# Kernel tuning notes

Measured on AMD Instinct MI355X. Metric: run time of the kernel, lower is better.

Reference implementation:

```python
import jax, jax.numpy as jnp
import numpy as np

B, S, D = 8, 2048, 64
NEG = -1e9


def setup_inputs() -> dict:
    key = jax.random.key(0)
    kq, kk, kv = jax.random.split(key, 3)
    return {
        "queries": jax.random.normal(kq, (B, S, D), dtype=jnp.float32),
        "keys": jax.random.normal(kk, (B, S, D), dtype=jnp.float32),
        "values": jax.random.normal(kv, (B, S, D), dtype=jnp.float32),
        "mask_q": jnp.ones((B, S), dtype=jnp.float32),
        "mask_k": jnp.ones((B, S), dtype=jnp.float32),
        "mask_v": jnp.ones((B, S), dtype=jnp.float32),
    }


def reference(queries, keys, values, mask_q, mask_k, mask_v):
    # scaled QK^T: [B, Sq, Sk]
    scaler = jnp.sqrt(jnp.asarray(queries.shape[-1], dtype=queries.dtype))
    scores = jnp.einsum("bqd,bkd->bqk", queries, keys) / scaler
    # additive padding mask from outer product of query/key masks
    padding_mask = mask_q[:, :, None] * mask_k[:, None, :]  # [B, Sq, Sk]
    scores = scores + (1.0 - padding_mask) * NEG
    attention_weights = jax.nn.softmax(scores, axis=-1)
    # mask values then weighted sum
    values = values * mask_v[:, :, None]
    output = jnp.einsum("bqk,bkd->bqd", attention_weights, values)
    return output
```

## Files before the change

### kernel.cpp

```cpp
#include <hip/hip_runtime.h>
#include <hip/hip_bf16.h>
#include <math.h>

#define BATCH 8
#define SEQ   2048
#define DIM   64
#define NEGC  (-1e9f)

typedef short short8 __attribute__((ext_vector_type(8)));
typedef float f32x4  __attribute__((ext_vector_type(4)));

#define MFMA(a, b, c) __builtin_amdgcn_mfma_f32_16x16x32_bf16((a), (b), (c), 0, 0, 0)

__device__ __forceinline__ ushort f2bf(float x) {
    uint u = __float_as_uint(x);
    uint r = (u + 0x7fffu + ((u >> 16) & 1u)) >> 16;
    return (ushort)r;
}
__device__ __forceinline__ float bf2f(ushort h) {
    return __uint_as_float(((uint)h) << 16);
}

__global__ __launch_bounds__(256)
void prep_kv(const float* __restrict__ K, const float* __restrict__ V,
             const float* __restrict__ MV, ushort* __restrict__ ws) {
    __shared__ float raw[64 * 68];
    const int t    = threadIdx.x;
    const int b    = blockIdx.x >> 5;
    const int tile = blockIdx.x & 31;
    const float* Kb  = K  + ((size_t)b * SEQ + tile * 64) * DIM;
    const float* Vb  = V  + ((size_t)b * SEQ + tile * 64) * DIM;
    const float* MVb = MV + (size_t)b * SEQ + tile * 64;
    ushort* wsI = ws + (size_t)(b * 32 + tile) * 8192;

#pragma unroll
    for (int u = 0; u < 4; u++) {
        int f = t + 256 * u, key = f >> 4, d4 = (f & 15) * 4;
        *(float4*)&raw[key * 68 + d4] = *(const float4*)(Kb + (size_t)f * 4);
    }
    __syncthreads();
#pragma unroll
    for (int u = 0; u < 2; u++) {
        int r = t + 256 * u;
        int mtc = r >> 6, qd = (r >> 4) & 3, mm = r & 15;
        int mt = mtc >> 1, c = mtc & 1;
        int key = mt * 16 + mm, d0 = c * 32 + qd * 8;
        float4 x0 = *(float4*)&raw[key * 68 + d0];
        float4 x1 = *(float4*)&raw[key * 68 + d0 + 4];
        float xs[8] = {x0.x, x0.y, x0.z, x0.w, x1.x, x1.y, x1.z, x1.w};
        short8 hv;
#pragma unroll
        for (int j = 0; j < 8; j++) hv[j] = (short)f2bf(xs[j]);
        *(short8*)(wsI + r * 8) = hv;
    }
    __syncthreads();

#pragma unroll
    for (int u = 0; u < 4; u++) {
        int f = t + 256 * u, key = f >> 4, d4 = (f & 15) * 4;
        float4 x = *(const float4*)(Vb + (size_t)f * 4);
        float mv = MVb[key];
        x.x *= mv; x.y *= mv; x.z *= mv; x.w *= mv;
        *(float4*)&raw[key * 68 + d4] = x;
    }
    __syncthreads();
#pragma unroll
    for (int u = 0; u < 2; u++) {
        int r = t + 256 * u;
        int kg5 = r >> 8, dg = (r >> 6) & 3, kq = (r >> 4) & 3, dm = r & 15;
        int d = dg * 16 + dm, k0 = kg5 * 32 + kq * 8;
        short8 ov;
#pragma unroll
        for (int j = 0; j < 8; j++) ov[j] = (short)f2bf(raw[(k0 + j) * 68 + d]);
        *(short8*)(wsI + 4096 + r * 8) = ov;
    }
}

__global__ __launch_bounds__(512, 2)
void attn_main(const float* __restrict__ Q, const float* __restrict__ MQ,
               const float* __restrict__ MK, const ushort* __restrict__ ws,
               float* __restrict__ O) {
    __shared__ __align__(16) ushort Stage[2][8192];
    __shared__ __align__(16) ushort Pf[8][512];
    __shared__ __align__(16) float  Msc[4][1280];

    const int t    = threadIdx.x;
    const int w    = t >> 6;
    const int lane = t & 63;
    const int quad = lane >> 4;
    const int lq   = lane & 15;
    const int qg   = w & 3;
    const int half = w >> 2;

    const int b  = blockIdx.x >> 5;
    const int q0 = (blockIdx.x & 31) * 64;
    const int q  = q0 + qg * 16 + lq;

    const float*  MKb = MK + (size_t)b * SEQ;
    const ushort* wsb = ws + (size_t)b * 32 * 8192;

    short8 qh[2], ql[2];
    {
        const float* Qr = Q + ((size_t)b * SEQ + q) * DIM;
#pragma unroll
        for (int c = 0; c < 2; c++) {
            float4 x0 = *(const float4*)(Qr + c * 32 + quad * 8);
            float4 x1 = *(const float4*)(Qr + c * 32 + quad * 8 + 4);
            float xs[8] = {x0.x, x0.y, x0.z, x0.w, x1.x, x1.y, x1.z, x1.w};
#pragma unroll
            for (int j = 0; j < 8; j++) {
                float v   = xs[j] * 0.125f;
                ushort hi = f2bf(v);
                ql[c][j]  = (short)f2bf(v - bf2f(hi));
                qh[c][j]  = (short)hi;
            }
        }
    }
    const float mq   = MQ[(size_t)b * SEQ + q];
    const float apen = NEGC * mq;

    float m = -1e30f, l = 0.0f;
    f32x4 ot0 = {0,0,0,0}, ot1 = {0,0,0,0}, ot2 = {0,0,0,0}, ot3 = {0,0,0,0};

    ushort* Pw   = Pf[w];
    const int kb = half * 32;

#pragma unroll
    for (int u = 0; u < 2; u++) {
        const int off = u * 4096 + w * 512;
        __builtin_amdgcn_global_load_lds(
            (const __attribute__((address_space(1))) void*)(wsb + off + lane * 8),
            (__attribute__((address_space(3))) void*)(&Stage[0][0] + off),
            16, 0, 0);
    }
    __syncthreads();

    f32x4 mkA = *(const f32x4*)(MKb + kb + quad * 4);
    f32x4 mkB = *(const f32x4*)(MKb + kb + 16 + quad * 4);

#pragma unroll 1
    for (int tile = 0; tile < 32; tile++) {
        const ushort* cur = &Stage[tile & 1][0];

        if (tile + 1 < 32) {
            const ushort* src = wsb + (size_t)(tile + 1) * 8192;
            ushort* dst = &Stage[(tile + 1) & 1][0];
#pragma unroll
            for (int u = 0; u < 2; u++) {
                const int off = u * 4096 + w * 512;
                __builtin_amdgcn_global_load_lds(
                    (const __attribute__((address_space(1))) void*)(src + off + lane * 8),
                    (__attribute__((address_space(3))) void*)(dst + off),
                    16, 0, 0);
            }
        }
        f32x4 nA = mkA, nB = mkB;
        if (tile + 1 < 32) {
            const float* mkp = MKb + (tile + 1) * 64 + kb + quad * 4;
            nA = *(const f32x4*)mkp;
            nB = *(const f32x4*)(mkp + 16);
        }

        f32x4 st0 = {0,0,0,0}, st1 = {0,0,0,0};
        const int mtg = half * 2;
#pragma unroll
        for (int c = 0; c < 2; c++) {
            short8 a0 = *(const short8*)&cur[((mtg + 0) * 2 + c) * 512 + lane * 8];
            short8 a1 = *(const short8*)&cur[((mtg + 1) * 2 + c) * 512 + lane * 8];
            st0 = MFMA(a0, qh[c], st0);
            st0 = MFMA(a0, ql[c], st0);
            st1 = MFMA(a1, qh[c], st1);
            st1 = MFMA(a1, ql[c], st1);
        }

        float s0[4], s1[4];
#pragma unroll
        for (int r = 0; r < 4; r++) {
            s0[r] = st0[r] + (NEGC - apen * mkA[r]);
            s1[r] = st1[r] + (NEGC - apen * mkB[r]);
        }
        float cm = s0[0];
#pragma unroll
        for (int r = 1; r < 4; r++) cm = fmaxf(cm, s0[r]);
#pragma unroll
        for (int r = 0; r < 4; r++) cm = fmaxf(cm, s1[r]);
        cm = fmaxf(cm, __shfl_xor(cm, 16));
        cm = fmaxf(cm, __shfl_xor(cm, 32));
        float nm    = fmaxf(m, cm);
        float alpha = __expf(m - nm);
        m = nm;

        float p0[4], p1[4], cs = 0.0f;
#pragma unroll
        for (int r = 0; r < 4; r++) { p0[r] = __expf(s0[r] - nm); cs += p0[r]; }
#pragma unroll
        for (int r = 0; r < 4; r++) { p1[r] = __expf(s1[r] - nm); cs += p1[r]; }
        cs += __shfl_xor(cs, 16);
        cs += __shfl_xor(cs, 32);
        l   = l * alpha + cs;
        ot0 *= alpha; ot1 *= alpha; ot2 *= alpha; ot3 *= alpha;

        __hip_bfloat162 c0 = __float22bfloat162_rn(make_float2(p0[0], p0[1]));
        __hip_bfloat162 c1 = __float22bfloat162_rn(make_float2(p0[2], p0[3]));
        __hip_bfloat162 c2 = __float22bfloat162_rn(make_float2(p1[0], p1[1]));
        __hip_bfloat162 c3 = __float22bfloat162_rn(make_float2(p1[2], p1[3]));
        uint2 pw0, pw1;
        __builtin_memcpy(&pw0.x, &c0, 4);
        __builtin_memcpy(&pw0.y, &c1, 4);
        __builtin_memcpy(&pw1.x, &c2, 4);
        __builtin_memcpy(&pw1.y, &c3, 4);
        int pidx0 = ((0 * 2 + (quad >> 1)) * 16 + lq) * 8 + (quad & 1) * 4;
        int pidx1 = ((1 * 2 + (quad >> 1)) * 16 + lq) * 8 + (quad & 1) * 4;
        *(uint2*)&Pw[pidx0] = pw0;
        *(uint2*)&Pw[pidx1] = pw1;
        short8 pfr = *(const short8*)&Pw[lane * 8];

        const ushort* VfC = cur + 4096;
        short8 v0 = *(const short8*)&VfC[(half * 4 + 0) * 512 + lane * 8];
        short8 v1 = *(const short8*)&VfC[(half * 4 + 1) * 512 + lane * 8];
        short8 v2 = *(const short8*)&VfC[(half * 4 + 2) * 512 + lane * 8];
        short8 v3 = *(const short8*)&VfC[(half * 4 + 3) * 512 + lane * 8];
        ot0 = MFMA(v0, pfr, ot0);
        ot1 = MFMA(v1, pfr, ot1);
        ot2 = MFMA(v2, pfr, ot2);
        ot3 = MFMA(v3, pfr, ot3);

        mkA = nA; mkB = nB;
        __syncthreads();
    }

    if (half == 1) {
        float* sc = &Msc[qg][lane * 20];
        *(f32x4*)&sc[0]  = ot0;
        *(f32x4*)&sc[4]  = ot1;
        *(f32x4*)&sc[8]  = ot2;
        *(f32x4*)&sc[12] = ot3;
        sc[16] = m;
        sc[17] = l;
    }
    __syncthreads();
    if (half == 0) {
        const float* sc = &Msc[qg][lane * 20];
        f32x4 ob0 = *(const f32x4*)&sc[0];
        f32x4 ob1 = *(const f32x4*)&sc[4];
        f32x4 ob2 = *(const f32x4*)&sc[8];
        f32x4 ob3 = *(const f32x4*)&sc[12];
        float mb = sc[16], lb = sc[17];

        float nm  = fmaxf(m, mb);
        float fa  = __expf(m - nm);
        float fb  = __expf(mb - nm);
        float inv = 1.0f / (l * fa + lb * fb);

        float* Orow = O + ((size_t)b * SEQ + q) * DIM;
        *(f32x4*)(Orow + 0  + quad * 4) = (ot0 * fa + ob0 * fb) * inv;
        *(f32x4*)(Orow + 16 + quad * 4) = (ot1 * fa + ob1 * fb) * inv;
        *(f32x4*)(Orow + 32 + quad * 4) = (ot2 * fa + ob2 * fb) * inv;
        *(f32x4*)(Orow + 48 + quad * 4) = (ot3 * fa + ob3 * fb) * inv;
    }
}

extern "C" void kernel_launch(void* const* d_in, const int* in_sizes, int n_in,
                              void* d_out, int out_size, void* d_ws, size_t ws_size,
                              hipStream_t stream) {
    const float* Q  = (const float*)d_in[0];
    const float* K  = (const float*)d_in[1];
    const float* V  = (const float*)d_in[2];
    const float* MQ = (const float*)d_in[3];
    const float* MK = (const float*)d_in[4];
    const float* MV = (const float*)d_in[5];
    float* O   = (float*)d_out;
    ushort* ws = (ushort*)d_ws;

    prep_kv<<<dim3(256), dim3(256), 0, stream>>>(K, V, MV, ws);
    attn_main<<<dim3(BATCH * (SEQ / 64)), dim3(512), 0, stream>>>(Q, MQ, MK, ws, O);
}
```

Before: 108.5 us.

## Switch to 32x32x16 MFMA, split keys across blocks, add merge kernel

```diff
diff --git a/kernel.cpp b/kernel.cpp
--- a/kernel.cpp
+++ b/kernel.cpp
@@ -7,10 +7,11 @@
 #define DIM   64
 #define NEGC  (-1e9f)
 
-typedef short short8 __attribute__((ext_vector_type(8)));
-typedef float f32x4  __attribute__((ext_vector_type(4)));
-
-#define MFMA(a, b, c) __builtin_amdgcn_mfma_f32_16x16x32_bf16((a), (b), (c), 0, 0, 0)
+typedef short short8  __attribute__((ext_vector_type(8)));
+typedef float f32x4   __attribute__((ext_vector_type(4)));
+typedef float f32x16  __attribute__((ext_vector_type(16)));
+
+#define MFMA32(a, b, c) __builtin_amdgcn_mfma_f32_32x32x16_bf16((a), (b), (c), 0, 0, 0)
 
 __device__ __forceinline__ ushort f2bf(float x) {
     uint u = __float_as_uint(x);
@@ -42,9 +43,8 @@
 #pragma unroll
     for (int u = 0; u < 2; u++) {
         int r = t + 256 * u;
-        int mtc = r >> 6, qd = (r >> 4) & 3, mm = r & 15;
-        int mt = mtc >> 1, c = mtc & 1;
-        int key = mt * 16 + mm, d0 = c * 32 + qd * 8;
+        int mt = r >> 8, kc = (r >> 6) & 3, L = r & 63;
+        int key = mt * 32 + (L & 31), d0 = kc * 16 + (L >> 5) * 8;
         float4 x0 = *(float4*)&raw[key * 68 + d0];
         float4 x1 = *(float4*)&raw[key * 68 + d0 + 4];
         float xs[8] = {x0.x, x0.y, x0.z, x0.w, x1.x, x1.y, x1.z, x1.w};
@@ -67,8 +67,8 @@
 #pragma unroll
     for (int u = 0; u < 2; u++) {
         int r = t + 256 * u;
-        int kg5 = r >> 8, dg = (r >> 6) & 3, kq = (r >> 4) & 3, dm = r & 15;
-        int d = dg * 16 + dm, k0 = kg5 * 32 + kq * 8;
+        int dt = r >> 8, kc = (r >> 6) & 3, L = r & 63;
+        int d = dt * 32 + (L & 31), k0 = kc * 16 + (L >> 5) * 8;
         short8 ov;
 #pragma unroll
         for (int j = 0; j < 8; j++) ov[j] = (short)f2bf(raw[(k0 + j) * 68 + d]);
@@ -76,43 +76,45 @@
     }
 }
 
-__global__ __launch_bounds__(512, 2)
+__global__ __launch_bounds__(256, 2)
 void attn_main(const float* __restrict__ Q, const float* __restrict__ MQ,
                const float* __restrict__ MK, const ushort* __restrict__ ws,
-               float* __restrict__ O) {
+               float* __restrict__ PO, float* __restrict__ ML) {
     __shared__ __align__(16) ushort Stage[2][8192];
-    __shared__ __align__(16) ushort Pf[8][512];
-    __shared__ __align__(16) float  Msc[4][1280];
+    __shared__ __align__(16) float  Msc[2][64 * 34];
 
     const int t    = threadIdx.x;
     const int w    = t >> 6;
     const int lane = t & 63;
-    const int quad = lane >> 4;
-    const int lq   = lane & 15;
-    const int qg   = w & 3;
-    const int half = w >> 2;
-
-    const int b  = blockIdx.x >> 5;
-    const int q0 = (blockIdx.x & 31) * 64;
-    const int q  = q0 + qg * 16 + lq;
-
-    const float*  MKb = MK + (size_t)b * SEQ;
-    const ushort* wsb = ws + (size_t)b * 32 * 8192;
-
-    short8 qh[2], ql[2];
+    const int h    = lane >> 5;
+    const int lm   = lane & 31;
+    const int qg   = w & 1;
+    const int kh   = w >> 1;
+
+    const int s  = blockIdx.x & 1;
+    const int qb = blockIdx.x >> 1;
+    const int b  = qb >> 5;
+    const int qt = qb & 31;
+    const int q  = qt * 64 + qg * 32 + lm;
+
+    const float*  MKb  = MK + (size_t)b * SEQ;
+    const ushort* wsKV = ws + (size_t)b * 32 * 8192;
+
+    short8 qh[4], ql[4];
     {
         const float* Qr = Q + ((size_t)b * SEQ + q) * DIM;
 #pragma unroll
-        for (int c = 0; c < 2; c++) {
-            float4 x0 = *(const float4*)(Qr + c * 32 + quad * 8);
-            float4 x1 = *(const float4*)(Qr + c * 32 + quad * 8 + 4);
+        for (int kc = 0; kc < 4; kc++) {
+            const float* p = Qr + kc * 16 + h * 8;
+            float4 x0 = *(const float4*)p;
+            float4 x1 = *(const float4*)(p + 4);
             float xs[8] = {x0.x, x0.y, x0.z, x0.w, x1.x, x1.y, x1.z, x1.w};
 #pragma unroll
             for (int j = 0; j < 8; j++) {
                 float v   = xs[j] * 0.125f;
                 ushort hi = f2bf(v);
-                ql[c][j]  = (short)f2bf(v - bf2f(hi));
-                qh[c][j]  = (short)hi;
+                ql[kc][j] = (short)f2bf(v - bf2f(hi));
+                qh[kc][j] = (short)hi;
             }
         }
     }
@@ -120,144 +122,181 @@
     const float apen = NEGC * mq;
 
     float m = -1e30f, l = 0.0f;
-    f32x4 ot0 = {0,0,0,0}, ot1 = {0,0,0,0}, ot2 = {0,0,0,0}, ot3 = {0,0,0,0};
-
-    ushort* Pw   = Pf[w];
-    const int kb = half * 32;
-
-#pragma unroll
-    for (int u = 0; u < 2; u++) {
-        const int off = u * 4096 + w * 512;
-        __builtin_amdgcn_global_load_lds(
-            (const __attribute__((address_space(1))) void*)(wsb + off + lane * 8),
-            (__attribute__((address_space(3))) void*)(&Stage[0][0] + off),
-            16, 0, 0);
-    }
-    __syncthreads();
-
-    f32x4 mkA = *(const f32x4*)(MKb + kb + quad * 4);
-    f32x4 mkB = *(const f32x4*)(MKb + kb + 16 + quad * 4);
+    f32x16 ot0, ot1;
+#pragma unroll
+    for (int i = 0; i < 16; i++) { ot0[i] = 0.0f; ot1[i] = 0.0f; }
+
+    {
+        const ushort* src = wsKV + (size_t)(s * 16) * 8192;
+#pragma unroll
+        for (int u = 0; u < 4; u++) {
+            const int off = (u * 256 + w * 64 + lane) * 8;
+            __builtin_amdgcn_global_load_lds(
+                (const __attribute__((address_space(1))) void*)(src + off),
+                (__attribute__((address_space(3))) void*)(&Stage[0][0] + off),
+                16, 0, 0);
+        }
+    }
+    __syncthreads();
+
+    f32x4 mk[4];
+#pragma unroll
+    for (int v = 0; v < 4; v++)
+        mk[v] = *(const f32x4*)(MKb + (s * 16) * 64 + kh * 32 + v * 8 + h * 4);
 
 #pragma unroll 1
-    for (int tile = 0; tile < 32; tile++) {
-        const ushort* cur = &Stage[tile & 1][0];
-
-        if (tile + 1 < 32) {
-            const ushort* src = wsb + (size_t)(tile + 1) * 8192;
-            ushort* dst = &Stage[(tile + 1) & 1][0];
-#pragma unroll
-            for (int u = 0; u < 2; u++) {
-                const int off = u * 4096 + w * 512;
+    for (int tt = 0; tt < 16; tt++) {
+        const ushort* cur = &Stage[tt & 1][0];
+
+        if (tt + 1 < 16) {
+            const ushort* src = wsKV + (size_t)(s * 16 + tt + 1) * 8192;
+            ushort* dst = &Stage[(tt + 1) & 1][0];
+#pragma unroll
+            for (int u = 0; u < 4; u++) {
+                const int off = (u * 256 + w * 64 + lane) * 8;
                 __builtin_amdgcn_global_load_lds(
-                    (const __attribute__((address_space(1))) void*)(src + off + lane * 8),
+                    (const __attribute__((address_space(1))) void*)(src + off),
                     (__attribute__((address_space(3))) void*)(dst + off),
                     16, 0, 0);
             }
         }
-        f32x4 nA = mkA, nB = mkB;
-        if (tile + 1 < 32) {
-            const float* mkp = MKb + (tile + 1) * 64 + kb + quad * 4;
-            nA = *(const f32x4*)mkp;
-            nB = *(const f32x4*)(mkp + 16);
-        }
-
-        f32x4 st0 = {0,0,0,0}, st1 = {0,0,0,0};
-        const int mtg = half * 2;
-#pragma unroll
-        for (int c = 0; c < 2; c++) {
-            short8 a0 = *(const short8*)&cur[((mtg + 0) * 2 + c) * 512 + lane * 8];
-            short8 a1 = *(const short8*)&cur[((mtg + 1) * 2 + c) * 512 + lane * 8];
-            st0 = MFMA(a0, qh[c], st0);
-            st0 = MFMA(a0, ql[c], st0);
-            st1 = MFMA(a1, qh[c], st1);
-            st1 = MFMA(a1, ql[c], st1);
-        }
-
-        float s0[4], s1[4];
-#pragma unroll
-        for (int r = 0; r < 4; r++) {
-            s0[r] = st0[r] + (NEGC - apen * mkA[r]);
-            s1[r] = st1[r] + (NEGC - apen * mkB[r]);
-        }
-        float cm = s0[0];
-#pragma unroll
-        for (int r = 1; r < 4; r++) cm = fmaxf(cm, s0[r]);
-#pragma unroll
-        for (int r = 0; r < 4; r++) cm = fmaxf(cm, s1[r]);
-        cm = fmaxf(cm, __shfl_xor(cm, 16));
+        f32x4 nmk[4];
+#pragma unroll
+        for (int v = 0; v < 4; v++) nmk[v] = mk[v];
+        if (tt + 1 < 16) {
+            const float* mkp = MKb + (s * 16 + tt + 1) * 64 + kh * 32 + h * 4;
+#pragma unroll
+            for (int v = 0; v < 4; v++) nmk[v] = *(const f32x4*)(mkp + v * 8);
+        }
+
+        f32x16 st;
+#pragma unroll
+        for (int i = 0; i < 16; i++) st[i] = 0.0f;
+#pragma unroll
+        for (int kc = 0; kc < 4; kc++) {
+            short8 a = *(const short8*)&cur[((kh * 4 + kc) * 64 + lane) * 8];
+            st = MFMA32(a, qh[kc], st);
+            st = MFMA32(a, ql[kc], st);
+        }
+
+        float sv[16];
+#pragma unroll
+        for (int v = 0; v < 4; v++)
+#pragma unroll
+            for (int c = 0; c < 4; c++)
+                sv[v * 4 + c] = st[v * 4 + c] + (NEGC - apen * mk[v][c]);
+        float cm = sv[0];
+#pragma unroll
+        for (int i = 1; i < 16; i++) cm = fmaxf(cm, sv[i]);
         cm = fmaxf(cm, __shfl_xor(cm, 32));
         float nm    = fmaxf(m, cm);
         float alpha = __expf(m - nm);
         m = nm;
 
-        float p0[4], p1[4], cs = 0.0f;
-#pragma unroll
-        for (int r = 0; r < 4; r++) { p0[r] = __expf(s0[r] - nm); cs += p0[r]; }
-#pragma unroll
-        for (int r = 0; r < 4; r++) { p1[r] = __expf(s1[r] - nm); cs += p1[r]; }
-        cs += __shfl_xor(cs, 16);
+        float p[16], cs = 0.0f;
+#pragma unroll
+        for (int i = 0; i < 16; i++) { p[i] = __expf(sv[i] - nm); cs += p[i]; }
         cs += __shfl_xor(cs, 32);
         l   = l * alpha + cs;
-        ot0 *= alpha; ot1 *= alpha; ot2 *= alpha; ot3 *= alpha;
-
-        __hip_bfloat162 c0 = __float22bfloat162_rn(make_float2(p0[0], p0[1]));
-        __hip_bfloat162 c1 = __float22bfloat162_rn(make_float2(p0[2], p0[3]));
-        __hip_bfloat162 c2 = __float22bfloat162_rn(make_float2(p1[0], p1[1]));
-        __hip_bfloat162 c3 = __float22bfloat162_rn(make_float2(p1[2], p1[3]));
-        uint2 pw0, pw1;
-        __builtin_memcpy(&pw0.x, &c0, 4);
-        __builtin_memcpy(&pw0.y, &c1, 4);
-        __builtin_memcpy(&pw1.x, &c2, 4);
-        __builtin_memcpy(&pw1.y, &c3, 4);
-        int pidx0 = ((0 * 2 + (quad >> 1)) * 16 + lq) * 8 + (quad & 1) * 4;
-        int pidx1 = ((1 * 2 + (quad >> 1)) * 16 + lq) * 8 + (quad & 1) * 4;
-        *(uint2*)&Pw[pidx0] = pw0;
-        *(uint2*)&Pw[pidx1] = pw1;
-        short8 pfr = *(const short8*)&Pw[lane * 8];
-
-        const ushort* VfC = cur + 4096;
-        short8 v0 = *(const short8*)&VfC[(half * 4 + 0) * 512 + lane * 8];
-        short8 v1 = *(const short8*)&VfC[(half * 4 + 1) * 512 + lane * 8];
-        short8 v2 = *(const short8*)&VfC[(half * 4 + 2) * 512 + lane * 8];
-        short8 v3 = *(const short8*)&VfC[(half * 4 + 3) * 512 + lane * 8];
-        ot0 = MFMA(v0, pfr, ot0);
-        ot1 = MFMA(v1, pfr, ot1);
-        ot2 = MFMA(v2, pfr, ot2);
-        ot3 = MFMA(v3, pfr, ot3);
-
-        mkA = nA; mkB = nB;
+        ot0 *= alpha; ot1 *= alpha;
+
+        uint g[4][2], x[4][2];
+#pragma unroll
+        for (int v = 0; v < 4; v++) {
+            __hip_bfloat162 c0 = __float22bfloat162_rn(make_float2(p[v*4+0], p[v*4+1]));
+            __hip_bfloat162 c1 = __float22bfloat162_rn(make_float2(p[v*4+2], p[v*4+3]));
+            __builtin_memcpy(&g[v][0], &c0, 4);
+            __builtin_memcpy(&g[v][1], &c1, 4);
+            x[v][0] = (uint)__shfl_xor((int)g[v][0], 32);
+            x[v][1] = (uint)__shfl_xor((int)g[v][1], 32);
+        }
+        uint pbw[2][4];
+        pbw[0][0] = h ? x[1][0] : g[0][0];
+        pbw[0][1] = h ? x[1][1] : g[0][1];
+        pbw[0][2] = h ? g[1][0] : x[0][0];
+        pbw[0][3] = h ? g[1][1] : x[0][1];
+        pbw[1][0] = h ? x[3][0] : g[2][0];
+        pbw[1][1] = h ? x[3][1] : g[2][1];
+        pbw[1][2] = h ? g[3][0] : x[2][0];
+        pbw[1][3] = h ? g[3][1] : x[2][1];
+
+#pragma unroll
+        for (int c = 0; c < 2; c++) {
+            short8 pb;
+            __builtin_memcpy(&pb, &pbw[c][0], 16);
+            short8 v0 = *(const short8*)&cur[4096 + ((0 * 4 + kh * 2 + c) * 64 + lane) * 8];
+            short8 v1 = *(const short8*)&cur[4096 + ((1 * 4 + kh * 2 + c) * 64 + lane) * 8];
+            ot0 = MFMA32(v0, pb, ot0);
+            ot1 = MFMA32(v1, pb, ot1);
+        }
+
+#pragma unroll
+        for (int v = 0; v < 4; v++) mk[v] = nmk[v];
         __syncthreads();
     }
 
-    if (half == 1) {
-        float* sc = &Msc[qg][lane * 20];
-        *(f32x4*)&sc[0]  = ot0;
-        *(f32x4*)&sc[4]  = ot1;
-        *(f32x4*)&sc[8]  = ot2;
-        *(f32x4*)&sc[12] = ot3;
-        sc[16] = m;
-        sc[17] = l;
-    }
-    __syncthreads();
-    if (half == 0) {
-        const float* sc = &Msc[qg][lane * 20];
-        f32x4 ob0 = *(const f32x4*)&sc[0];
-        f32x4 ob1 = *(const f32x4*)&sc[4];
-        f32x4 ob2 = *(const f32x4*)&sc[8];
-        f32x4 ob3 = *(const f32x4*)&sc[12];
-        float mb = sc[16], lb = sc[17];
-
-        float nm  = fmaxf(m, mb);
-        float fa  = __expf(m - nm);
-        float fb  = __expf(mb - nm);
-        float inv = 1.0f / (l * fa + lb * fb);
-
-        float* Orow = O + ((size_t)b * SEQ + q) * DIM;
-        *(f32x4*)(Orow + 0  + quad * 4) = (ot0 * fa + ob0 * fb) * inv;
-        *(f32x4*)(Orow + 16 + quad * 4) = (ot1 * fa + ob1 * fb) * inv;
-        *(f32x4*)(Orow + 32 + quad * 4) = (ot2 * fa + ob2 * fb) * inv;
-        *(f32x4*)(Orow + 48 + quad * 4) = (ot3 * fa + ob3 * fb) * inv;
-    }
+    if (kh == 1) {
+        float* sc = &Msc[qg][lane * 34];
+#pragma unroll
+        for (int i = 0; i < 16; i++) { sc[i] = ot0[i]; sc[16 + i] = ot1[i]; }
+        sc[32] = m;
+        sc[33] = l;
+    }
+    __syncthreads();
+    if (kh == 0) {
+        const float* sc = &Msc[qg][lane * 34];
+        float mb = sc[32], lb = sc[33];
+        float nm = fmaxf(m, mb);
+        float fa = __expf(m - nm);
+        float fb = __expf(mb - nm);
+        float lt = l * fa + lb * fb;
+
+        float* po = PO + (((size_t)(s * 8 + b) * 32 + qt) * 64 + qg * 32 + lm) * 64;
+#pragma unroll
+        for (int dt = 0; dt < 2; dt++) {
+            const f32x16& o = dt ? ot1 : ot0;
+#pragma unroll
+            for (int rq = 0; rq < 4; rq++) {
+                f32x4 r;
+#pragma unroll
+                for (int c = 0; c < 4; c++)
+                    r[c] = o[rq * 4 + c] * fa + sc[dt * 16 + rq * 4 + c] * fb;
+                *(f32x4*)(po + dt * 32 + rq * 8 + h * 4) = r;
+            }
+        }
+        if (h == 0) {
+            float2* ml2 = (float2*)ML;
+            ml2[((size_t)(s * 8 + b) * 32 + qt) * 64 + qg * 32 + lm] =
+                make_float2(nm, lt);
+        }
+    }
+}
+
+__global__ __launch_bounds__(256)
+void merge_o(const float* __restrict__ PO, const float* __restrict__ ML,
+             float* __restrict__ O) {
+    const int tid = blockIdx.x * 256 + threadIdx.x;
+    const int qln = tid >> 4;
+    const int dq  = tid & 15;
+    const int b   = qln >> 11;
+    const int qr  = qln & 2047;
+    const int qt  = qr >> 6;
+    const int qq  = qr & 63;
+
+    const float2* ml2 = (const float2*)ML;
+    const size_t mlidx = ((size_t)b * 32 + qt) * 64 + qq;
+    float2 A = ml2[mlidx];
+    float2 Bv = ml2[(size_t)8 * 32 * 64 + mlidx];
+    float mm = fmaxf(A.x, Bv.x);
+    float fa = __expf(A.x - mm);
+    float fb = __expf(Bv.x - mm);
+    float inv = 1.0f / (A.y * fa + Bv.y * fb);
+
+    const size_t o0 = (((size_t)b * 32 + qt) * 64 + qq) * 64 + dq * 4;
+    f32x4 va = *(const f32x4*)(PO + o0);
+    f32x4 vb = *(const f32x4*)(PO + (size_t)8 * 32 * 64 * 64 + o0);
+    f32x4 r = (va * fa + vb * fb) * inv;
+    *(f32x4*)(O + ((size_t)b * SEQ + qr) * DIM + dq * 4) = r;
 }
 
 extern "C" void kernel_launch(void* const* d_in, const int* in_sizes, int n_in,
@@ -269,9 +308,13 @@
     const float* MQ = (const float*)d_in[3];
     const float* MK = (const float*)d_in[4];
     const float* MV = (const float*)d_in[5];
-    float* O   = (float*)d_out;
-    ushort* ws = (ushort*)d_ws;
-
-    prep_kv<<<dim3(256), dim3(256), 0, stream>>>(K, V, MV, ws);
-    attn_main<<<dim3(BATCH * (SEQ / 64)), dim3(512), 0, stream>>>(Q, MQ, MK, ws, O);
-}
+    float* O = (float*)d_out;
+
+    ushort* wsKV = (ushort*)d_ws;
+    float*  PO   = (float*)((char*)d_ws + (4u << 20));
+    float*  ML   = (float*)((char*)d_ws + (12u << 20));
+
+    prep_kv  <<<dim3(256),  dim3(256), 0, stream>>>(K, V, MV, wsKV);
+    attn_main<<<dim3(512),  dim3(256), 0, stream>>>(Q, MQ, MK, wsKV, PO, ML);
+    merge_o  <<<dim3(1024), dim3(256), 0, stream>>>(PO, ML, O);
+}
```

After: 101.7 us. 1.07x faster.
